# Optimization experiments

Hardware: AMD Instinct MI355X
Metric: run time of the kernel (lower is better)

The kernel has to match this reference:

```python
import jax, jax.numpy as jnp
import numpy as np

N_NODES = 50000
N_EDGES = 1600000
N_REL = 8
D_IN = 128
D_HID = 128
D_OUT = 64
N_POOL = 256


def setup_inputs() -> dict:
    key = jax.random.key(0)
    ks = jax.random.split(key, 10)
    x = jax.random.uniform(ks[0], (N_NODES, D_IN), dtype=jnp.float32)
    edge_index = jax.random.randint(ks[1], (2, N_EDGES), 0, N_NODES)
    edge_type = jax.random.randint(ks[2], (N_EDGES,), 0, N_REL)
    pool_indices = jax.random.randint(ks[3], (N_POOL,), 0, N_NODES)
    s1 = 1.0 / np.sqrt(D_IN)
    s2 = 1.0 / np.sqrt(D_HID)
    W1 = jax.random.normal(ks[4], (N_REL, D_IN, D_HID), dtype=jnp.float32) * s1
    root1 = jax.random.normal(ks[5], (D_IN, D_HID), dtype=jnp.float32) * s1
    b1 = jnp.zeros((D_HID,), jnp.float32)
    W2 = jax.random.normal(ks[6], (N_REL, D_HID, D_OUT), dtype=jnp.float32) * s2
    root2 = jax.random.normal(ks[7], (D_HID, D_OUT), dtype=jnp.float32) * s2
    b2 = jnp.zeros((D_OUT,), jnp.float32)
    return {"x": x, "edge_index": edge_index, "edge_type": edge_type,
            "pool_indices": pool_indices, "W1": W1, "root1": root1, "b1": b1,
            "W2": W2, "root2": root2, "b2": b2}


def rgcn_layer(h, edge_index, edge_type, W, root, b):
    # PyG RGCNConv: out = h @ root + sum_r mean_{j in N_r(i)} (h_j @ W_r) + b
    src, dst = edge_index[0], edge_index[1]
    n = h.shape[0]
    r = W.shape[0]
    hW = jnp.einsum('nd,rdh->rnh', h, W)          # (R, N, H)
    msg = hW[edge_type, src]                      # (E, H) gather per edge
    seg = edge_type * n + dst                     # per-(relation, dst) segment
    agg = jax.ops.segment_sum(msg, seg, num_segments=r * n)
    agg = agg.reshape(r, n, -1)
    cnt = jax.ops.segment_sum(jnp.ones(msg.shape[0], h.dtype), seg,
                              num_segments=r * n).reshape(r, n, 1)
    mean = agg / jnp.maximum(cnt, 1.0)            # per-relation mean
    return mean.sum(0) + h @ root + b


def reference(x, edge_index, edge_type, pool_indices, W1, root1, b1, W2, root2, b2):
    h = jax.nn.relu(rgcn_layer(x, edge_index, edge_type, W1, root1, b1))
    node_embeddings = rgcn_layer(h, edge_index, edge_type, W2, root2, b2)
    selected_embeddings = node_embeddings[pool_indices]       # (P, D_OUT)
    type_features = x[pool_indices, :3]                       # (P, 3)
    weights = jnp.array([4.0, 1.0, 2.0], dtype=x.dtype)
    entity_weights = type_features @ weights                  # (P,)
    sum_of_weights = jnp.sum(entity_weights) + 1e-9
    pooled = jnp.sum(selected_embeddings * entity_weights[:, None], axis=0,
                     keepdims=True) / sum_of_weights          # (1, D_OUT)
    return pooled
```

## Files before the change

kernel.cpp:

```cpp
#include <hip/hip_runtime.h>

#define N_NODES 50000
#define N_EDGES 1600000
#define N_REL   8
#define D_IN    128
#define D_HID   128
#define D_OUT   64
#define N_POOL  256

#define CAP_S   12288
#define BUCKET  32
#define BUCKET2 32
#define NSEG_N  (N_REL * N_NODES)

typedef short v8s __attribute__((ext_vector_type(8)));
typedef float v4f __attribute__((ext_vector_type(4)));

constexpr size_t OFF_FILLC  = 0;
constexpr size_t OFF_FILLC2 = OFF_FILLC + NSEG_N;
constexpr size_t ZERO_ELEMS = OFF_FILLC2 + NSEG_N;
constexpr size_t OFF_PBIT   = ZERO_ELEMS;
constexpr size_t OFF_SBIT   = OFF_PBIT + 2048;
constexpr size_t OFF_CTR    = OFF_SBIT + 2048;
constexpr size_t OFF_SNODES = OFF_CTR + 16;
constexpr size_t OFF_SRCSLOT= OFF_SNODES + CAP_S;
constexpr size_t OFF_ESLOT2 = OFF_SRCSLOT + (size_t)NSEG_N * BUCKET;
constexpr size_t OFF_AGG1B  = OFF_ESLOT2 + (size_t)NSEG_N * BUCKET2;
constexpr size_t OFF_XALL   = OFF_AGG1B + (size_t)NSEG_N * 64;
constexpr size_t OFF_WT     = OFF_XALL + (size_t)N_NODES * 64;
constexpr size_t OFF_H      = OFF_WT + (size_t)1152 * 128 / 2;
constexpr size_t OFF_EMB    = OFF_H + (size_t)N_NODES * D_HID;
constexpr size_t TOTAL_ELEMS= OFF_EMB + (size_t)N_POOL * D_OUT;

__device__ __forceinline__ unsigned short f2bf(float f) {
  union { float f; unsigned u; } v; v.f = f;
  unsigned r = v.u + 0x7FFFu + ((v.u >> 16) & 1u);
  return (unsigned short)(r >> 16);
}
__device__ __forceinline__ float bfLo(unsigned v) { return __uint_as_float(v << 16); }
__device__ __forceinline__ float bfHi(unsigned v) { return __uint_as_float(v & 0xFFFF0000u); }

__global__ __launch_bounds__(256) void k_init(
    const int* __restrict__ pool, const float* __restrict__ x,
    const float* __restrict__ W1, const float* __restrict__ root1,
    float* __restrict__ ws) {
  unsigned* pBit = (unsigned*)(ws + OFF_PBIT);
  unsigned* sBit = (unsigned*)(ws + OFF_SBIT);
  int*      ctr  = (int*)(ws + OFF_CTR);
  unsigned long long* xall8 = (unsigned long long*)(ws + OFF_XALL);
  unsigned short* Wt = (unsigned short*)(ws + OFF_WT);
  float4*   emb4 = (float4*)(ws + OFF_EMB);
  int tid = threadIdx.x, bid = blockIdx.x;
  int gtid = bid * 256 + tid, gthr = gridDim.x * 256;
  int wave = tid >> 6, lane = tid & 63;

  float4 z = {0.f, 0.f, 0.f, 0.f};
  for (int i = gtid; i < (int)(ZERO_ELEMS / 4); i += gthr) ((float4*)ws)[i] = z;
  for (int i = gtid; i < N_POOL * D_OUT / 4; i += gthr) emb4[i] = z;

  if (bid == 0) {
    for (int i = tid; i < 2048; i += 256) { pBit[i] = 0u; sBit[i] = 0u; }
    if (tid < 16) ctr[tid] = 0;
    __syncthreads();
    int node = pool[tid];
    unsigned bit = 1u << (node & 31);
    atomicOr(&pBit[node >> 5], bit);
    atomicOr(&sBit[node >> 5], bit);
  }

  int gw = (bid - 1) * 4 + wave;
  if (bid >= 1 && gw < 288) {
    int kt = gw >> 3, nt = gw & 7;
    int k0 = kt * 32 + ((lane >> 4) << 3);
    int n = nt * 16 + (lane & 15);
    v8s frag;
#pragma unroll
    for (int j = 0; j < 8; j++) {
      int kg = k0 + j;
      float v = (kg < 1024) ? W1[(size_t)kg * D_HID + n]
                            : root1[(size_t)(kg - 1024) * D_HID + n];
      frag[j] = (short)f2bf(v);
    }
    ((v8s*)Wt)[gw * 64 + lane] = frag;
  }

  for (int i = gtid; i < N_NODES * 32; i += gthr) {
    float4 v = ((const float4*)x)[i];
    unsigned lo = ((unsigned)f2bf(v.y) << 16) | f2bf(v.x);
    unsigned hi = ((unsigned)f2bf(v.w) << 16) | f2bf(v.z);
    xall8[i] = (unsigned long long)lo | ((unsigned long long)hi << 32);
  }
}

__global__ __launch_bounds__(256) void k_pass1(
    const int* __restrict__ EI, const int* __restrict__ pool,
    unsigned* __restrict__ sBit) {
  __shared__ unsigned pb[2048];
  int tid = threadIdx.x;
  for (int i = tid; i < 2048; i += 256) pb[i] = 0u;
  __syncthreads();
  { int node = pool[tid]; atomicOr(&pb[node >> 5], 1u << (node & 31)); }
  __syncthreads();
  int idx = blockIdx.x * 256 + tid;
  if (idx >= N_EDGES / 4) return;
  int4 d4 = ((const int4*)(EI + N_EDGES))[idx];
  int d[4] = {d4.x, d4.y, d4.z, d4.w};
#pragma unroll
  for (int i = 0; i < 4; i++) {
    int dst = d[i];
    if ((pb[dst >> 5] >> (dst & 31)) & 1u) {
      int src = EI[idx * 4 + i];
      atomicOr(&sBit[src >> 5], 1u << (src & 31));
    }
  }
}

__global__ __launch_bounds__(256) void k_fillc(
    const int* __restrict__ EI, const int* __restrict__ ET,
    const int* __restrict__ pool, const unsigned* __restrict__ sBit,
    int* __restrict__ fillCtr, int* __restrict__ srcSlot,
    int* __restrict__ fillCtr2, int* __restrict__ eslot2,
    int* __restrict__ sNodes, int* __restrict__ ctr) {
  __shared__ unsigned pb[2048];
  __shared__ int ismem[8];
  int tid = threadIdx.x, bid = blockIdx.x;
  int wave = tid >> 6, lane = tid & 63;
  for (int i = tid; i < 2048; i += 256) pb[i] = 0u;
  __syncthreads();
  { int node = pool[tid]; atomicOr(&pb[node >> 5], 1u << (node & 31)); }
  __syncthreads();

  if (bid < 196) {
    int node = bid * 256 + tid;
    bool sp = (node < N_NODES) && ((sBit[node >> 5] >> (node & 31)) & 1u);
    unsigned long long m = __ballot(sp);
    if (lane == 0) ismem[wave] = __popcll(m);
    __syncthreads();
    if (tid == 0) {
      int tot = ismem[0] + ismem[1] + ismem[2] + ismem[3];
      ismem[4] = tot ? atomicAdd(&ctr[1], tot) : 0;
    }
    __syncthreads();
    if (sp) {
      int off = ismem[4];
      for (int w2 = 0; w2 < wave; w2++) off += ismem[w2];
      int id = off + __popcll(m & ((1ull << lane) - 1ull));
      if (id < CAP_S) sNodes[id] = node;
    }
  }

  int idx = bid * 256 + tid;
  if (idx >= N_EDGES / 4) return;
  int4 d4 = ((const int4*)(EI + N_EDGES))[idx];
  int d[4] = {d4.x, d4.y, d4.z, d4.w};
  bool any = false;
#pragma unroll
  for (int i = 0; i < 4; i++)
    any |= ((sBit[d[i] >> 5] >> (d[i] & 31)) & 1u) != 0u;
  if (!any) return;
  int4 t4 = ((const int4*)ET)[idx];
  int4 s4 = ((const int4*)EI)[idx];
  int t[4] = {t4.x, t4.y, t4.z, t4.w};
  int s[4] = {s4.x, s4.y, s4.z, s4.w};
#pragma unroll
  for (int i = 0; i < 4; i++) {
    int dst = d[i];
    if ((sBit[dst >> 5] >> (dst & 31)) & 1u) {
      int seg = (dst << 3) + t[i];
      int slot = atomicAdd(&fillCtr[seg], 1);
      if (slot < BUCKET) srcSlot[(size_t)seg * BUCKET + slot] = s[i];
      if ((pb[dst >> 5] >> (dst & 31)) & 1u) {
        int slot2 = atomicAdd(&fillCtr2[seg], 1);
        if (slot2 < BUCKET2) eslot2[(size_t)seg * BUCKET2 + slot2] = s[i];
      }
    }
  }
}

__global__ __launch_bounds__(256) void k_gather(
    const int* __restrict__ fillCtr, const int* __restrict__ srcSlot,
    const unsigned long long* __restrict__ xall8, const int* __restrict__ ctr,
    const int* __restrict__ sNodes, unsigned long long* __restrict__ agg1b8) {
  int sCount = ctr[1]; if (sCount > CAP_S) sCount = CAP_S;
  int total = sCount << 3;
  int lane = threadIdx.x & 63;
  int half = lane >> 5, hl = lane & 31;
  int wstride = gridDim.x << 2;
  for (int p = (blockIdx.x << 2) + (threadIdx.x >> 6); 2 * p < total; p += wstride) {
    int w = 2 * p + half;
    if (w < total) {
      int node = sNodes[w >> 3];
      int seg = (node << 3) + (w & 7);
      int cnt = fillCtr[seg];
      if (cnt > BUCKET) cnt = BUCKET;
      const int* slot = srcSlot + (size_t)seg * BUCKET;
      float a0 = 0.f, a1 = 0.f, a2 = 0.f, a3 = 0.f;
      int i = 0;
      for (; i + 4 <= cnt; i += 4) {
        int s0 = slot[i + 0];
        int s1 = slot[i + 1];
        int s2 = slot[i + 2];
        int s3 = slot[i + 3];
        unsigned long long v0 = xall8[(size_t)s0 * 32 + hl];
        unsigned long long v1 = xall8[(size_t)s1 * 32 + hl];
        unsigned long long v2 = xall8[(size_t)s2 * 32 + hl];
        unsigned long long v3 = xall8[(size_t)s3 * 32 + hl];
        unsigned l0 = (unsigned)v0, h0 = (unsigned)(v0 >> 32);
        unsigned l1 = (unsigned)v1, h1 = (unsigned)(v1 >> 32);
        unsigned l2 = (unsigned)v2, h2 = (unsigned)(v2 >> 32);
        unsigned l3 = (unsigned)v3, h3 = (unsigned)(v3 >> 32);
        a0 += (bfLo(l0) + bfLo(l1)) + (bfLo(l2) + bfLo(l3));
        a1 += (bfHi(l0) + bfHi(l1)) + (bfHi(l2) + bfHi(l3));
        a2 += (bfLo(h0) + bfLo(h1)) + (bfLo(h2) + bfLo(h3));
        a3 += (bfHi(h0) + bfHi(h1)) + (bfHi(h2) + bfHi(h3));
      }
      for (; i < cnt; i++) {
        unsigned long long v = xall8[(size_t)slot[i] * 32 + hl];
        unsigned lo = (unsigned)v, hi = (unsigned)(v >> 32);
        a0 += bfLo(lo); a1 += bfHi(lo);
        a2 += bfLo(hi); a3 += bfHi(hi);
      }
      float inv = 1.0f / fmaxf((float)cnt, 1.0f);
      unsigned w0 = ((unsigned)f2bf(a1 * inv) << 16) | f2bf(a0 * inv);
      unsigned w1 = ((unsigned)f2bf(a3 * inv) << 16) | f2bf(a2 * inv);
      agg1b8[(size_t)seg * 32 + hl] =
          (unsigned long long)w0 | ((unsigned long long)w1 << 32);
    }
  }
}

__global__ __launch_bounds__(256) void k_gemm1(
    const unsigned* __restrict__ agg1b, const unsigned* __restrict__ xall,
    const unsigned short* __restrict__ Wt, const float* __restrict__ b1,
    const int* __restrict__ sNodes, const int* __restrict__ ctr,
    float* __restrict__ h) {
  int sCount = ctr[1]; if (sCount > CAP_S) sCount = CAP_S;
  int s0 = blockIdx.x * 16;
  if (s0 >= sCount) return;
  int wave = threadIdx.x >> 6, lane = threadIdx.x & 63;
  int quad = lane >> 4, mn = lane & 15;
  int srow = s0 + mn;
  int g = (srow < sCount) ? sNodes[srow] : 0;
  v4f acc0 = (v4f){0.f, 0.f, 0.f, 0.f};
  v4f acc1 = (v4f){0.f, 0.f, 0.f, 0.f};
  const v8s* WtF = (const v8s*)Wt;
  for (int kt = 0; kt < 36; kt++) {
    const unsigned short* aptr;
    if (kt < 32) {
      int r = kt >> 2;
      int d0 = (kt & 3) * 32 + quad * 8;
      aptr = (const unsigned short*)agg1b + ((size_t)((g << 3) + r) * 128 + d0);
    } else {
      int d0 = (kt - 32) * 32 + quad * 8;
      aptr = (const unsigned short*)xall + ((size_t)g * 128 + d0);
    }
    v8s afrag = *(const v8s*)aptr;
    const v8s* wrow = WtF + (size_t)(kt * 8 + wave * 2) * 64 + lane;
    acc0 = __builtin_amdgcn_mfma_f32_16x16x32_bf16(afrag, wrow[0],  acc0, 0, 0, 0);
    acc1 = __builtin_amdgcn_mfma_f32_16x16x32_bf16(afrag, wrow[64], acc1, 0, 0, 0);
  }
  int col0 = wave * 32 + mn;
  int col1 = col0 + 16;
  float bv0 = b1[col0], bv1 = b1[col1];
#pragma unroll
  for (int reg = 0; reg < 4; reg++) {
    int s = s0 + quad * 4 + reg;
    if (s < sCount) {
      int gh = sNodes[s];
      h[(size_t)gh * D_HID + col0] = fmaxf(acc0[reg] + bv0, 0.0f);
      h[(size_t)gh * D_HID + col1] = fmaxf(acc1[reg] + bv1, 0.0f);
    }
  }
}

__global__ __launch_bounds__(256) void k_gemmB(
    const float* __restrict__ x, const int* __restrict__ pool,
    const float* __restrict__ W2, const float* __restrict__ root2,
    const float* __restrict__ b2, const int* __restrict__ fillCtr2,
    const int* __restrict__ eslot2, int* __restrict__ ctr,
    const float* __restrict__ h, float* __restrict__ emb,
    float* __restrict__ out) {
  __shared__ float smem[896];
  __shared__ int lastFlag;
  int tid = threadIdx.x, wave = tid >> 6, lane = tid & 63;
  int pl = blockIdx.x >> 1, half = blockIdx.x & 1;
  {
    int nodeP = pool[pl];
    float* a = smem;
    float* partial = smem + 640;
    int r = half * 4 + wave;
    int code = (nodeP << 3) + r;
    int cnt = fillCtr2[code]; if (cnt > BUCKET2) cnt = BUCKET2;
    const int* sl = eslot2 + (size_t)code * BUCKET2;
    float s0 = 0.f, s1 = 0.f;
    for (int i = 0; i < cnt; i++) {
      float2 v = ((const float2*)h)[(size_t)sl[i] * 64 + lane];
      s0 += v.x; s1 += v.y;
    }
    float inv = 1.0f / fmaxf((float)cnt, 1.0f);
    a[wave * 128 + lane * 2]     = s0 * inv;
    a[wave * 128 + lane * 2 + 1] = s1 * inv;
    if (half == 1 && tid < 128) a[512 + tid] = h[(size_t)nodeP * D_HID + tid];
    __syncthreads();
    float acc = 0.0f;
    int kbase = half * 512 + wave * 128;
#pragma unroll 8
    for (int j = 0; j < 128; j++)
      acc += a[wave * 128 + j] * W2[(size_t)(kbase + j) * D_OUT + lane];
    if (half == 1) {
      int rbase = wave * 32;
#pragma unroll 4
      for (int j = 0; j < 32; j++)
        acc += a[512 + rbase + j] * root2[(size_t)(rbase + j) * D_OUT + lane];
    }
    partial[tid] = acc;
    __syncthreads();
    if (tid < 64) {
      float r4 = partial[tid] + partial[tid + 64] + partial[tid + 128] + partial[tid + 192];
      if (half == 0) r4 += b2[tid];
      unsafeAtomicAdd(&emb[(size_t)pl * D_OUT + tid], r4);
    }
  }
  __syncthreads();
  if (tid == 0) {
    __builtin_amdgcn_fence(__ATOMIC_RELEASE, "agent");
    int old = __hip_atomic_fetch_add(&ctr[2], 1, __ATOMIC_RELAXED,
                                     __HIP_MEMORY_SCOPE_AGENT);
    lastFlag = (old == (int)gridDim.x - 1) ? 1 : 0;
  }
  __syncthreads();
  if (lastFlag == 0) return;
  if (tid == 0) __builtin_amdgcn_fence(__ATOMIC_ACQUIRE, "agent");
  __syncthreads();
  {
    float* ew  = smem;
    float* part= smem + 512;
    int node = pool[tid];
    const float* xr = x + (size_t)node * D_IN;
    ew[tid] = 4.0f * xr[0] + 1.0f * xr[1] + 2.0f * xr[2];
    __syncthreads();
    float acc = 0.0f;
    int j0 = wave * 64;
#pragma unroll 8
    for (int j = j0; j < j0 + 64; j++)
      acc += ew[j] * emb[(size_t)j * D_OUT + lane];
    part[wave * 64 + lane] = acc;
    __syncthreads();
    if (tid < 64) {
      float sw = 0.0f;
      for (int j = 0; j < N_POOL; j++) sw += ew[j];
      float r4 = part[tid] + part[64 + tid] + part[128 + tid] + part[192 + tid];
      out[tid] = r4 / (sw + 1e-9f);
    }
  }
}

extern "C" void kernel_launch(void* const* d_in, const int* in_sizes, int n_in,
                              void* d_out, int out_size, void* d_ws, size_t ws_size,
                              hipStream_t stream) {
  const float* x     = (const float*)d_in[0];
  const int*   EI    = (const int*)  d_in[1];
  const int*   ET    = (const int*)  d_in[2];
  const int*   pool  = (const int*)  d_in[3];
  const float* W1    = (const float*)d_in[4];
  const float* root1 = (const float*)d_in[5];
  const float* b1    = (const float*)d_in[6];
  const float* W2    = (const float*)d_in[7];
  const float* root2 = (const float*)d_in[8];
  const float* b2    = (const float*)d_in[9];
  float* out = (float*)d_out;
  float* ws  = (float*)d_ws;

  int*      fillCtr = (int*)(ws + OFF_FILLC);
  int*      fillCtr2= (int*)(ws + OFF_FILLC2);
  unsigned* sBit    = (unsigned*)(ws + OFF_SBIT);
  int*      ctr     = (int*)(ws + OFF_CTR);
  int*      sNodes  = (int*)(ws + OFF_SNODES);
  int*      srcSlot = (int*)(ws + OFF_SRCSLOT);
  int*      eslot2  = (int*)(ws + OFF_ESLOT2);
  unsigned* agg1b   = (unsigned*)(ws + OFF_AGG1B);
  unsigned* xall    = (unsigned*)(ws + OFF_XALL);
  unsigned short* Wt = (unsigned short*)(ws + OFF_WT);
  float*    h       = ws + OFF_H;
  float*    emb     = ws + OFF_EMB;

  k_init<<<1024, 256, 0, stream>>>(pool, x, W1, root1, ws);
  k_pass1<<<(N_EDGES / 4 + 255) / 256, 256, 0, stream>>>(EI, pool, sBit);
  k_fillc<<<(N_EDGES / 4 + 255) / 256, 256, 0, stream>>>(
      EI, ET, pool, sBit, fillCtr, srcSlot, fillCtr2, eslot2, sNodes, ctr);
  k_gather<<<4096, 256, 0, stream>>>(
      fillCtr, srcSlot, (const unsigned long long*)xall, ctr, sNodes,
      (unsigned long long*)agg1b);
  k_gemm1<<<CAP_S / 16, 256, 0, stream>>>(agg1b, xall, Wt, b1, sNodes, ctr, h);
  k_gemmB<<<2 * N_POOL, 256, 0, stream>>>(
      x, pool, W2, root2, b2, fillCtr2, eslot2, ctr, h, emb, out);
}
```

Before: 176.0 us.

## Index layer-1 outputs by compact node id and reuse first-hop buckets

Drops the separate second-hop slot table and its counters, since pool-node segments already sit in the main bucket table (pool nodes are in the S set). The layer-1 aggregate buffer and hidden-state array are now indexed by compact S-set ids instead of global node ids, through a new node-to-id map, which shrinks the zeroed region and the workspace footprint and improves locality. This removes extra atomics and scattered writes in the fill kernel. In exchange the layer-2 gather takes an extra indirection through the id map.

```diff
diff --git a/kernel.cpp b/kernel.cpp
--- a/kernel.cpp
+++ b/kernel.cpp
@@ -10,26 +10,24 @@
 
 #define CAP_S   12288
 #define BUCKET  32
-#define BUCKET2 32
 #define NSEG_N  (N_REL * N_NODES)
 
 typedef short v8s __attribute__((ext_vector_type(8)));
 typedef float v4f __attribute__((ext_vector_type(4)));
 
 constexpr size_t OFF_FILLC  = 0;
-constexpr size_t OFF_FILLC2 = OFF_FILLC + NSEG_N;
-constexpr size_t ZERO_ELEMS = OFF_FILLC2 + NSEG_N;
+constexpr size_t ZERO_ELEMS = NSEG_N;
 constexpr size_t OFF_PBIT   = ZERO_ELEMS;
 constexpr size_t OFF_SBIT   = OFF_PBIT + 2048;
 constexpr size_t OFF_CTR    = OFF_SBIT + 2048;
 constexpr size_t OFF_SNODES = OFF_CTR + 16;
-constexpr size_t OFF_SRCSLOT= OFF_SNODES + CAP_S;
-constexpr size_t OFF_ESLOT2 = OFF_SRCSLOT + (size_t)NSEG_N * BUCKET;
-constexpr size_t OFF_AGG1B  = OFF_ESLOT2 + (size_t)NSEG_N * BUCKET2;
-constexpr size_t OFF_XALL   = OFF_AGG1B + (size_t)NSEG_N * 64;
+constexpr size_t OFF_SID    = OFF_SNODES + CAP_S;
+constexpr size_t OFF_SRCSLOT= OFF_SID + N_NODES;
+constexpr size_t OFF_AGG1B  = OFF_SRCSLOT + (size_t)NSEG_N * BUCKET;
+constexpr size_t OFF_XALL   = OFF_AGG1B + (size_t)CAP_S * 8 * 64;
 constexpr size_t OFF_WT     = OFF_XALL + (size_t)N_NODES * 64;
 constexpr size_t OFF_H      = OFF_WT + (size_t)1152 * 128 / 2;
-constexpr size_t OFF_EMB    = OFF_H + (size_t)N_NODES * D_HID;
+constexpr size_t OFF_EMB    = OFF_H + (size_t)CAP_S * D_HID;
 constexpr size_t TOTAL_ELEMS= OFF_EMB + (size_t)N_POOL * D_OUT;
 
 __device__ __forceinline__ unsigned short f2bf(float f) {
@@ -117,18 +115,12 @@
 
 __global__ __launch_bounds__(256) void k_fillc(
     const int* __restrict__ EI, const int* __restrict__ ET,
-    const int* __restrict__ pool, const unsigned* __restrict__ sBit,
+    const unsigned* __restrict__ sBit,
     int* __restrict__ fillCtr, int* __restrict__ srcSlot,
-    int* __restrict__ fillCtr2, int* __restrict__ eslot2,
-    int* __restrict__ sNodes, int* __restrict__ ctr) {
-  __shared__ unsigned pb[2048];
+    int* __restrict__ sNodes, int* __restrict__ sId, int* __restrict__ ctr) {
   __shared__ int ismem[8];
   int tid = threadIdx.x, bid = blockIdx.x;
   int wave = tid >> 6, lane = tid & 63;
-  for (int i = tid; i < 2048; i += 256) pb[i] = 0u;
-  __syncthreads();
-  { int node = pool[tid]; atomicOr(&pb[node >> 5], 1u << (node & 31)); }
-  __syncthreads();
 
   if (bid < 196) {
     int node = bid * 256 + tid;
@@ -145,7 +137,7 @@
       int off = ismem[4];
       for (int w2 = 0; w2 < wave; w2++) off += ismem[w2];
       int id = off + __popcll(m & ((1ull << lane) - 1ull));
-      if (id < CAP_S) sNodes[id] = node;
+      if (id < CAP_S) { sNodes[id] = node; sId[node] = id; }
     }
   }
 
@@ -169,10 +161,6 @@
       int seg = (dst << 3) + t[i];
       int slot = atomicAdd(&fillCtr[seg], 1);
       if (slot < BUCKET) srcSlot[(size_t)seg * BUCKET + slot] = s[i];
-      if ((pb[dst >> 5] >> (dst & 31)) & 1u) {
-        int slot2 = atomicAdd(&fillCtr2[seg], 1);
-        if (slot2 < BUCKET2) eslot2[(size_t)seg * BUCKET2 + slot2] = s[i];
-      }
     }
   }
 }
@@ -223,7 +211,7 @@
       float inv = 1.0f / fmaxf((float)cnt, 1.0f);
       unsigned w0 = ((unsigned)f2bf(a1 * inv) << 16) | f2bf(a0 * inv);
       unsigned w1 = ((unsigned)f2bf(a3 * inv) << 16) | f2bf(a2 * inv);
-      agg1b8[(size_t)seg * 32 + hl] =
+      agg1b8[(size_t)w * 32 + hl] =
           (unsigned long long)w0 | ((unsigned long long)w1 << 32);
     }
   }
@@ -249,7 +237,7 @@
     if (kt < 32) {
       int r = kt >> 2;
       int d0 = (kt & 3) * 32 + quad * 8;
-      aptr = (const unsigned short*)agg1b + ((size_t)((g << 3) + r) * 128 + d0);
+      aptr = (const unsigned short*)agg1b + ((size_t)((srow << 3) + r) * 128 + d0);
     } else {
       int d0 = (kt - 32) * 32 + quad * 8;
       aptr = (const unsigned short*)xall + ((size_t)g * 128 + d0);
@@ -266,9 +254,8 @@
   for (int reg = 0; reg < 4; reg++) {
     int s = s0 + quad * 4 + reg;
     if (s < sCount) {
-      int gh = sNodes[s];
-      h[(size_t)gh * D_HID + col0] = fmaxf(acc0[reg] + bv0, 0.0f);
-      h[(size_t)gh * D_HID + col1] = fmaxf(acc1[reg] + bv1, 0.0f);
+      h[(size_t)s * D_HID + col0] = fmaxf(acc0[reg] + bv0, 0.0f);
+      h[(size_t)s * D_HID + col1] = fmaxf(acc1[reg] + bv1, 0.0f);
     }
   }
 }
@@ -276,10 +263,10 @@
 __global__ __launch_bounds__(256) void k_gemmB(
     const float* __restrict__ x, const int* __restrict__ pool,
     const float* __restrict__ W2, const float* __restrict__ root2,
-    const float* __restrict__ b2, const int* __restrict__ fillCtr2,
-    const int* __restrict__ eslot2, int* __restrict__ ctr,
-    const float* __restrict__ h, float* __restrict__ emb,
-    float* __restrict__ out) {
+    const float* __restrict__ b2, const int* __restrict__ fillCtr,
+    const int* __restrict__ srcSlot, const int* __restrict__ sId,
+    int* __restrict__ ctr, const float* __restrict__ h,
+    float* __restrict__ emb, float* __restrict__ out) {
   __shared__ float smem[896];
   __shared__ int lastFlag;
   int tid = threadIdx.x, wave = tid >> 6, lane = tid & 63;
@@ -289,18 +276,22 @@
     float* a = smem;
     float* partial = smem + 640;
     int r = half * 4 + wave;
-    int code = (nodeP << 3) + r;
-    int cnt = fillCtr2[code]; if (cnt > BUCKET2) cnt = BUCKET2;
-    const int* sl = eslot2 + (size_t)code * BUCKET2;
+    int seg = (nodeP << 3) + r;
+    int cnt = fillCtr[seg]; if (cnt > BUCKET) cnt = BUCKET;
+    const int* sl = srcSlot + (size_t)seg * BUCKET;
     float s0 = 0.f, s1 = 0.f;
     for (int i = 0; i < cnt; i++) {
-      float2 v = ((const float2*)h)[(size_t)sl[i] * 64 + lane];
+      int row = sId[sl[i]];
+      float2 v = ((const float2*)h)[(size_t)row * 64 + lane];
       s0 += v.x; s1 += v.y;
     }
     float inv = 1.0f / fmaxf((float)cnt, 1.0f);
     a[wave * 128 + lane * 2]     = s0 * inv;
     a[wave * 128 + lane * 2 + 1] = s1 * inv;
-    if (half == 1 && tid < 128) a[512 + tid] = h[(size_t)nodeP * D_HID + tid];
+    if (half == 1 && tid < 128) {
+      int rowP = sId[nodeP];
+      a[512 + tid] = h[(size_t)rowP * D_HID + tid];
+    }
     __syncthreads();
     float acc = 0.0f;
     int kbase = half * 512 + wave * 128;
@@ -372,12 +363,11 @@
   float* ws  = (float*)d_ws;
 
   int*      fillCtr = (int*)(ws + OFF_FILLC);
-  int*      fillCtr2= (int*)(ws + OFF_FILLC2);
   unsigned* sBit    = (unsigned*)(ws + OFF_SBIT);
   int*      ctr     = (int*)(ws + OFF_CTR);
   int*      sNodes  = (int*)(ws + OFF_SNODES);
+  int*      sId     = (int*)(ws + OFF_SID);
   int*      srcSlot = (int*)(ws + OFF_SRCSLOT);
-  int*      eslot2  = (int*)(ws + OFF_ESLOT2);
   unsigned* agg1b   = (unsigned*)(ws + OFF_AGG1B);
   unsigned* xall    = (unsigned*)(ws + OFF_XALL);
   unsigned short* Wt = (unsigned short*)(ws + OFF_WT);
@@ -387,11 +377,11 @@
   k_init<<<1024, 256, 0, stream>>>(pool, x, W1, root1, ws);
   k_pass1<<<(N_EDGES / 4 + 255) / 256, 256, 0, stream>>>(EI, pool, sBit);
   k_fillc<<<(N_EDGES / 4 + 255) / 256, 256, 0, stream>>>(
-      EI, ET, pool, sBit, fillCtr, srcSlot, fillCtr2, eslot2, sNodes, ctr);
+      EI, ET, sBit, fillCtr, srcSlot, sNodes, sId, ctr);
   k_gather<<<4096, 256, 0, stream>>>(
       fillCtr, srcSlot, (const unsigned long long*)xall, ctr, sNodes,
       (unsigned long long*)agg1b);
   k_gemm1<<<CAP_S / 16, 256, 0, stream>>>(agg1b, xall, Wt, b1, sNodes, ctr, h);
   k_gemmB<<<2 * N_POOL, 256, 0, stream>>>(
-      x, pool, W2, root2, b2, fillCtr2, eslot2, ctr, h, emb, out);
-}
+      x, pool, W2, root2, b2, fillCtr, srcSlot, sId, ctr, h, emb, out);
+}
```

After: 176.0 us. No clear change (-0.0%).
